# Kernel optimization log

Measured on AMD Instinct MI355X. Metric: run time of the kernel, lower is better.

The kernel has to match this reference:

```python
import jax, jax.numpy as jnp
import numpy as np
from jax import lax


def setup_inputs() -> dict:
    key = jax.random.key(0)
    k1, k2, k3, k4 = jax.random.split(key, 4)
    D = 128
    B = 16
    image = jax.random.normal(k1, (1, D, D, D), jnp.float32)          # [1, D, H, W]
    x = jax.random.normal(k2, (B, 1, D, D, D), jnp.float32)           # [B, 1, D, H, W]
    # Conv3d(1, 27, kernel_size=3) parameters
    W = jax.random.normal(k3, (27, 1, 3, 3, 3), jnp.float32) * (1.0 / np.sqrt(27.0))
    b = jax.random.normal(k4, (27,), jnp.float32) * 0.01
    return {"image": image, "x": x, "W": W, "b": b}


def reference(image, x, W, b):
    D, H, Wd = image.shape[1], image.shape[2], image.shape[3]
    # K = Conv3d(image): per-voxel 27 filter taps. Unbatched CDHW -> add batch dim.
    K = lax.conv_general_dilated(
        image[None], W, window_strides=(1, 1, 1), padding='SAME',
        dimension_numbers=('NCDHW', 'OIDHW', 'NCDHW'))[0]             # [27, D, H, W]
    K = K + b[:, None, None, None]
    # permute (1,2,3,0) + unflatten(3,(3,3,3)) -> [D, H, W, 3, 3, 3]
    K = jnp.moveaxis(K, 0, -1).reshape(D, H, Wd, 3, 3, 3)
    # Apply dynamic per-voxel 3x3x3 filter: sum of 27 shifted slices
    xp = jnp.pad(x, ((0, 0), (0, 0), (1, 1), (1, 1), (1, 1)))         # [B,1,D+2,H+2,W+2]
    y = jnp.zeros_like(x)
    for di in range(3):
        for dj in range(3):
            for dk in range(3):
                tap = K[..., di, dj, dk][None, None]                  # [1,1,D,H,W]
                y = y + tap * xp[:, :, di:di + D, dj:dj + H, dk:dk + Wd]
    return y
```

## Files before the change

### kernel.cpp

```cpp
#include <hip/hip_runtime.h>

typedef __fp16 f16x2 __attribute__((ext_vector_type(2)));

#define Dm 128
#define Bn 16
#define VOX (Dm * Dm * Dm)
#define NT 256
#define WR 10
#define SLAB 320

__device__ __forceinline__ int iclamp(int v, int lo, int hi) {
  return v < lo ? lo : (v > hi ? hi : v);
}
__device__ __forceinline__ f16x2 pkrtz(float lo, float hi) {
  return __builtin_amdgcn_cvt_pkrtz(lo, hi);
}
__device__ __forceinline__ float pkbits(float lo, float hi) {
  return __builtin_bit_cast(float, __builtin_amdgcn_cvt_pkrtz(lo, hi));
}
__device__ __forceinline__ f16x2 asf16x2(float w) {
  return __builtin_bit_cast(f16x2, w);
}
__device__ __forceinline__ f16x2 midpair(f16x2 P, f16x2 Q) {
  unsigned r = __builtin_amdgcn_perm(__builtin_bit_cast(unsigned, P),
                                     __builtin_bit_cast(unsigned, Q),
                                     0x05040302u);
  return __builtin_bit_cast(f16x2, r);
}

extern "C" __global__ void packW(const float* __restrict__ Wf,
                                 const float* __restrict__ bfp,
                                 float* __restrict__ wpk) {
  int i = threadIdx.x;
  if (i < 729) {
    int o = i / 27, t = i - o * 27;
    float v = Wf[i];
    wpk[t * 27 + o] = pkbits(v, v);
  } else if (i < 756) {
    float b = bfp[i - 729];
    wpk[i] = pkbits(b, b);
  }
}

__device__ __forceinline__ void load_batch(float2 nx[5], const float* xb,
                                           const int off[5]) {
#pragma unroll
  for (int k = 0; k < 5; ++k) nx[k] = *(const float2*)(xb + off[k]);
}
__device__ __forceinline__ void stage_lds(float* sxw, const float2 nx[5],
                                          int lane) {
#pragma unroll
  for (int k = 0; k < 5; ++k)
    sxw[64 * k + lane] = pkbits(nx[k].x, nx[k].y);
}
__device__ __forceinline__ f16x2 apply_tile(const float* sxw, const f16x2* K2,
                                            int ty, int tx) {
  f16x2 aA = {(__fp16)0.f, (__fp16)0.f};
  f16x2 aB = {(__fp16)0.f, (__fp16)0.f};
#pragma unroll
  for (int rr = 0; rr < 9; ++rr) {
    const int idx = ((rr / 3) * 10 + ty + (rr % 3)) * WR + tx;
    f16x2 a2 = asf16x2(sxw[idx]);
    f16x2 b2 = asf16x2(sxw[idx + 1]);
    f16x2 c2 = asf16x2(sxw[idx + 2]);
    f16x2 h01 = midpair(b2, a2);
    f16x2 h12 = b2;
    f16x2 h23 = midpair(c2, b2);
    if (rr & 1) {
      aB = __builtin_elementwise_fma(K2[rr * 3 + 0], h01, aB);
      aB = __builtin_elementwise_fma(K2[rr * 3 + 1], h12, aB);
      aB = __builtin_elementwise_fma(K2[rr * 3 + 2], h23, aB);
    } else {
      aA = __builtin_elementwise_fma(K2[rr * 3 + 0], h01, aA);
      aA = __builtin_elementwise_fma(K2[rr * 3 + 1], h12, aA);
      aA = __builtin_elementwise_fma(K2[rr * 3 + 2], h23, aA);
    }
  }
  return aA + aB;
}

extern "C" __global__ void __launch_bounds__(NT, 4)
fused3d(const float* __restrict__ img, const float* __restrict__ x,
        const float* __restrict__ wpk, float* __restrict__ out)
{
  __shared__ float sImg[4][SLAB];
  __shared__ float sX0[4][SLAB];
  __shared__ float sX1[4][SLAB];

  const int tid  = threadIdx.x;
  const int lane = tid & 63;
  const int wv   = tid >> 6;
  const int tx   = lane & 7;
  const int ty   = lane >> 3;

  const int bid = blockIdx.x;
  const int s  = (bid & 7) * 512 + (bid >> 3);
  const int bx = s & 7, by = (s >> 3) & 15, bz = s >> 7;
  const int w0 = bx * 16, h0 = by * 8, d0 = bz * 4;

  int off[5];
  float mk0[5], mk1[5];
#pragma unroll
  for (int k = 0; k < 5; ++k) {
    int i  = 64 * k + lane;
    int r  = i / WR;
    int c  = i - r * WR;
    int zz = r / 10;
    int yy = r - zz * 10;
    int gdo = d0 + wv + zz - 1;
    int gho = h0 + yy - 1;
    int gwo = w0 - 2 + 2 * c;
    int gd = iclamp(gdo, 0, Dm - 1);
    int gh = iclamp(gho, 0, Dm - 1);
    int gw = iclamp(gwo, 0, Dm - 2);
    off[k] = (gd * Dm + gh) * Dm + gw;
    bool rk = ((unsigned)gdo < Dm) & ((unsigned)gho < Dm);
    mk0[k] = (rk & ((unsigned)gwo < Dm))       ? 1.f : 0.f;
    mk1[k] = (rk & ((unsigned)(gwo + 1) < Dm)) ? 1.f : 0.f;
  }

  float* simg = sImg[wv];
  float* sx0  = sX0[wv];
  float* sx1  = sX1[wv];

  float2 nxA[5], nxB[5];
  load_batch(nxA, x, off);
#pragma unroll
  for (int k = 0; k < 5; ++k) {
    float2 v = *(const float2*)(img + off[k]);
    simg[64 * k + lane] = pkbits(v.x * mk0[k], v.y * mk1[k]);
  }

  f16x2 K2[27];
#pragma unroll
  for (int o = 0; o < 27; ++o) K2[o] = asf16x2(wpk[729 + o]);
#pragma unroll
  for (int rr = 0; rr < 9; ++rr) {
    const int idx = ((rr / 3) * 10 + ty + (rr % 3)) * WR + tx;
    f16x2 a2 = asf16x2(simg[idx]);
    f16x2 b2 = asf16x2(simg[idx + 1]);
    f16x2 c2 = asf16x2(simg[idx + 2]);
    f16x2 h01 = midpair(b2, a2);
    f16x2 h12 = b2;
    f16x2 h23 = midpair(c2, b2);
    const float* wA = wpk + (rr * 3 + 0) * 27;
    const float* wB = wpk + (rr * 3 + 1) * 27;
    const float* wC = wpk + (rr * 3 + 2) * 27;
#pragma unroll
    for (int o = 0; o < 27; ++o) {
      K2[o] = __builtin_elementwise_fma(asf16x2(wA[o]), h01, K2[o]);
      K2[o] = __builtin_elementwise_fma(asf16x2(wB[o]), h12, K2[o]);
      K2[o] = __builtin_elementwise_fma(asf16x2(wC[o]), h23, K2[o]);
    }
  }

  const int od = d0 + wv, oh = h0 + ty, ow = w0 + 2 * tx;
#pragma unroll
  for (int o = 0; o < 27; ++o) {
    const int di = o / 9, dj = (o / 3) % 3, dk = o % 3;
    const bool mm = ((unsigned)(od + di - 1) < Dm) & ((unsigned)(oh + dj - 1) < Dm);
    const float m0 = (mm & ((unsigned)(ow + dk - 1) < Dm)) ? 1.f : 0.f;
    const float m1 = (mm & ((unsigned)(ow + dk)     < Dm)) ? 1.f : 0.f;
    K2[o] *= pkrtz(m0, m1);
  }

  const size_t obase = (((size_t)od) * Dm + oh) * Dm + ow;

#pragma unroll 1
  for (int bb = 0; bb < Bn; bb += 2) {
    stage_lds(sx0, nxA, lane);
    load_batch(nxB, x + (size_t)(bb + 1) * VOX, off);
    {
      f16x2 acc = apply_tile(sx0, K2, ty, tx);
      float2 st; st.x = (float)acc.x; st.y = (float)acc.y;
      *(float2*)&out[(size_t)bb * VOX + obase] = st;
    }
    stage_lds(sx1, nxB, lane);
    if (bb + 2 < Bn) load_batch(nxA, x + (size_t)(bb + 2) * VOX, off);
    {
      f16x2 acc = apply_tile(sx1, K2, ty, tx);
      float2 st; st.x = (float)acc.x; st.y = (float)acc.y;
      *(float2*)&out[(size_t)(bb + 1) * VOX + obase] = st;
    }
  }
}

extern "C" void kernel_launch(void* const* d_in, const int* in_sizes, int n_in,
                              void* d_out, int out_size, void* d_ws, size_t ws_size,
                              hipStream_t stream) {
  const float* img = (const float*)d_in[0];
  const float* x   = (const float*)d_in[1];
  const float* Wf  = (const float*)d_in[2];
  const float* bf  = (const float*)d_in[3];
  float* out = (float*)d_out;
  float* wpk = (float*)d_ws;
  hipLaunchKernelGGL(packW, dim3(1), dim3(768), 0, stream, Wf, bf, wpk);
  hipLaunchKernelGGL(fused3d, dim3(4096), dim3(NT), 0, stream, img, x, wpk, out);
}
```

Before: 122.2 us.

## Compute four output voxels per thread with wider tiles and float4 stores

Each thread now produces four consecutive W outputs instead of two, so the block tile widens to 32 and the grid is halved. Per-thread dynamic kernels double to two register sets (KA, KB), sharing LDS loads and midpair shuffles across both pairs. The image slab LDS buffer is dropped and sX0 is reused for the initial K computation. The aim is fewer LDS reads per output and wider stores, at the cost of higher register pressure (54 packed kernel registers plus 9 prefetch float2 per buffer) and less parallelism.

```diff
diff --git a/kernel.cpp b/kernel.cpp
--- a/kernel.cpp
+++ b/kernel.cpp
@@ -6,8 +6,9 @@
 #define Bn 16
 #define VOX (Dm * Dm * Dm)
 #define NT 256
-#define WR 10
-#define SLAB 320
+#define WR 19
+#define SLAB 589
+#define NSL 9
 
 __device__ __forceinline__ int iclamp(int v, int lo, int hi) {
   return v < lo ? lo : (v > hi ? hi : v);
@@ -42,48 +43,56 @@
   }
 }
 
-__device__ __forceinline__ void load_batch(float2 nx[5], const float* xb,
-                                           const int off[5]) {
-#pragma unroll
-  for (int k = 0; k < 5; ++k) nx[k] = *(const float2*)(xb + off[k]);
-}
-__device__ __forceinline__ void stage_lds(float* sxw, const float2 nx[5],
+__device__ __forceinline__ void load_batch(float2 nx[NSL], const float* xb,
+                                           const int off[NSL]) {
+#pragma unroll
+  for (int k = 0; k < NSL; ++k) nx[k] = *(const float2*)(xb + off[k]);
+}
+__device__ __forceinline__ void stage_lds(float* sxw, const float2 nx[NSL],
                                           int lane) {
 #pragma unroll
-  for (int k = 0; k < 5; ++k)
+  for (int k = 0; k < NSL; ++k)
     sxw[64 * k + lane] = pkbits(nx[k].x, nx[k].y);
 }
-__device__ __forceinline__ f16x2 apply_tile(const float* sxw, const f16x2* K2,
-                                            int ty, int tx) {
-  f16x2 aA = {(__fp16)0.f, (__fp16)0.f};
-  f16x2 aB = {(__fp16)0.f, (__fp16)0.f};
+
+__device__ __forceinline__ void apply_tile4(const float* sxw,
+                                            const f16x2* KA, const f16x2* KB,
+                                            int ty, int tx,
+                                            f16x2& outA, f16x2& outB) {
+  f16x2 aAa = {(__fp16)0.f, (__fp16)0.f}, aAb = aAa;
+  f16x2 aBa = aAa, aBb = aAa;
 #pragma unroll
   for (int rr = 0; rr < 9; ++rr) {
-    const int idx = ((rr / 3) * 10 + ty + (rr % 3)) * WR + tx;
-    f16x2 a2 = asf16x2(sxw[idx]);
-    f16x2 b2 = asf16x2(sxw[idx + 1]);
-    f16x2 c2 = asf16x2(sxw[idx + 2]);
-    f16x2 h01 = midpair(b2, a2);
-    f16x2 h12 = b2;
-    f16x2 h23 = midpair(c2, b2);
+    const int idx = ((rr / 3) * 10 + ty + (rr % 3)) * WR + 2 * tx;
+    float u0 = sxw[idx], u1 = sxw[idx + 1], u2 = sxw[idx + 2], u3 = sxw[idx + 3];
+    f16x2 h1 = asf16x2(u1), h2 = asf16x2(u2);
+    f16x2 m01 = midpair(h1, asf16x2(u0));
+    f16x2 m12 = midpair(h2, h1);
+    f16x2 m23 = midpair(asf16x2(u3), h2);
     if (rr & 1) {
-      aB = __builtin_elementwise_fma(K2[rr * 3 + 0], h01, aB);
-      aB = __builtin_elementwise_fma(K2[rr * 3 + 1], h12, aB);
-      aB = __builtin_elementwise_fma(K2[rr * 3 + 2], h23, aB);
+      aAb = __builtin_elementwise_fma(KA[rr * 3 + 0], m01, aAb);
+      aAb = __builtin_elementwise_fma(KA[rr * 3 + 1], h1,  aAb);
+      aAb = __builtin_elementwise_fma(KA[rr * 3 + 2], m12, aAb);
+      aBb = __builtin_elementwise_fma(KB[rr * 3 + 0], m12, aBb);
+      aBb = __builtin_elementwise_fma(KB[rr * 3 + 1], h2,  aBb);
+      aBb = __builtin_elementwise_fma(KB[rr * 3 + 2], m23, aBb);
     } else {
-      aA = __builtin_elementwise_fma(K2[rr * 3 + 0], h01, aA);
-      aA = __builtin_elementwise_fma(K2[rr * 3 + 1], h12, aA);
-      aA = __builtin_elementwise_fma(K2[rr * 3 + 2], h23, aA);
-    }
-  }
-  return aA + aB;
+      aAa = __builtin_elementwise_fma(KA[rr * 3 + 0], m01, aAa);
+      aAa = __builtin_elementwise_fma(KA[rr * 3 + 1], h1,  aAa);
+      aAa = __builtin_elementwise_fma(KA[rr * 3 + 2], m12, aAa);
+      aBa = __builtin_elementwise_fma(KB[rr * 3 + 0], m12, aBa);
+      aBa = __builtin_elementwise_fma(KB[rr * 3 + 1], h2,  aBa);
+      aBa = __builtin_elementwise_fma(KB[rr * 3 + 2], m23, aBa);
+    }
+  }
+  outA = aAa + aAb;
+  outB = aBa + aBb;
 }
 
 extern "C" __global__ void __launch_bounds__(NT, 4)
 fused3d(const float* __restrict__ img, const float* __restrict__ x,
         const float* __restrict__ wpk, float* __restrict__ out)
 {
-  __shared__ float sImg[4][SLAB];
   __shared__ float sX0[4][SLAB];
   __shared__ float sX1[4][SLAB];
 
@@ -94,14 +103,14 @@
   const int ty   = lane >> 3;
 
   const int bid = blockIdx.x;
-  const int s  = (bid & 7) * 512 + (bid >> 3);
-  const int bx = s & 7, by = (s >> 3) & 15, bz = s >> 7;
-  const int w0 = bx * 16, h0 = by * 8, d0 = bz * 4;
-
-  int off[5];
-  float mk0[5], mk1[5];
-#pragma unroll
-  for (int k = 0; k < 5; ++k) {
+  const int s  = (bid & 7) * 256 + (bid >> 3);
+  const int bx = s & 3, by = (s >> 2) & 15, bz = s >> 6;
+  const int w0 = bx * 32, h0 = by * 8, d0 = bz * 4;
+
+  int off[NSL];
+  float mk0[NSL], mk1[NSL];
+#pragma unroll
+  for (int k = 0; k < NSL; ++k) {
     int i  = 64 * k + lane;
     int r  = i / WR;
     int c  = i - r * WR;
@@ -114,73 +123,82 @@
     int gh = iclamp(gho, 0, Dm - 1);
     int gw = iclamp(gwo, 0, Dm - 2);
     off[k] = (gd * Dm + gh) * Dm + gw;
-    bool rk = ((unsigned)gdo < Dm) & ((unsigned)gho < Dm);
+    bool rk = ((unsigned)gdo < Dm) & ((unsigned)gho < Dm) & (zz < 3);
     mk0[k] = (rk & ((unsigned)gwo < Dm))       ? 1.f : 0.f;
     mk1[k] = (rk & ((unsigned)(gwo + 1) < Dm)) ? 1.f : 0.f;
   }
 
-  float* simg = sImg[wv];
-  float* sx0  = sX0[wv];
-  float* sx1  = sX1[wv];
-
-  float2 nxA[5], nxB[5];
+  float* sx0 = sX0[wv];
+  float* sx1 = sX1[wv];
+
+  float2 nxA[NSL], nxB[NSL];
   load_batch(nxA, x, off);
 #pragma unroll
-  for (int k = 0; k < 5; ++k) {
+  for (int k = 0; k < NSL; ++k) {
     float2 v = *(const float2*)(img + off[k]);
-    simg[64 * k + lane] = pkbits(v.x * mk0[k], v.y * mk1[k]);
-  }
-
-  f16x2 K2[27];
-#pragma unroll
-  for (int o = 0; o < 27; ++o) K2[o] = asf16x2(wpk[729 + o]);
+    sx0[64 * k + lane] = pkbits(v.x * mk0[k], v.y * mk1[k]);
+  }
+
+  f16x2 KA[27], KB[27];
+#pragma unroll
+  for (int o = 0; o < 27; ++o) { KA[o] = asf16x2(wpk[729 + o]); KB[o] = KA[o]; }
 #pragma unroll
   for (int rr = 0; rr < 9; ++rr) {
-    const int idx = ((rr / 3) * 10 + ty + (rr % 3)) * WR + tx;
-    f16x2 a2 = asf16x2(simg[idx]);
-    f16x2 b2 = asf16x2(simg[idx + 1]);
-    f16x2 c2 = asf16x2(simg[idx + 2]);
-    f16x2 h01 = midpair(b2, a2);
-    f16x2 h12 = b2;
-    f16x2 h23 = midpair(c2, b2);
+    const int idx = ((rr / 3) * 10 + ty + (rr % 3)) * WR + 2 * tx;
+    float u0 = sx0[idx], u1 = sx0[idx + 1], u2 = sx0[idx + 2], u3 = sx0[idx + 3];
+    f16x2 h1 = asf16x2(u1), h2 = asf16x2(u2);
+    f16x2 m01 = midpair(h1, asf16x2(u0));
+    f16x2 m12 = midpair(h2, h1);
+    f16x2 m23 = midpair(asf16x2(u3), h2);
     const float* wA = wpk + (rr * 3 + 0) * 27;
     const float* wB = wpk + (rr * 3 + 1) * 27;
     const float* wC = wpk + (rr * 3 + 2) * 27;
 #pragma unroll
     for (int o = 0; o < 27; ++o) {
-      K2[o] = __builtin_elementwise_fma(asf16x2(wA[o]), h01, K2[o]);
-      K2[o] = __builtin_elementwise_fma(asf16x2(wB[o]), h12, K2[o]);
-      K2[o] = __builtin_elementwise_fma(asf16x2(wC[o]), h23, K2[o]);
-    }
-  }
-
-  const int od = d0 + wv, oh = h0 + ty, ow = w0 + 2 * tx;
+      f16x2 wa = asf16x2(wA[o]), wb = asf16x2(wB[o]), wc = asf16x2(wC[o]);
+      KA[o] = __builtin_elementwise_fma(wa, m01, KA[o]);
+      KA[o] = __builtin_elementwise_fma(wb, h1,  KA[o]);
+      KA[o] = __builtin_elementwise_fma(wc, m12, KA[o]);
+      KB[o] = __builtin_elementwise_fma(wa, m12, KB[o]);
+      KB[o] = __builtin_elementwise_fma(wb, h2,  KB[o]);
+      KB[o] = __builtin_elementwise_fma(wc, m23, KB[o]);
+    }
+  }
+
+  const int od = d0 + wv, oh = h0 + ty, ow = w0 + 4 * tx;
 #pragma unroll
   for (int o = 0; o < 27; ++o) {
     const int di = o / 9, dj = (o / 3) % 3, dk = o % 3;
     const bool mm = ((unsigned)(od + di - 1) < Dm) & ((unsigned)(oh + dj - 1) < Dm);
-    const float m0 = (mm & ((unsigned)(ow + dk - 1) < Dm)) ? 1.f : 0.f;
-    const float m1 = (mm & ((unsigned)(ow + dk)     < Dm)) ? 1.f : 0.f;
-    K2[o] *= pkrtz(m0, m1);
+    const float a0 = (mm & ((unsigned)(ow + dk - 1) < Dm)) ? 1.f : 0.f;
+    const float a1 = (mm & ((unsigned)(ow + dk)     < Dm)) ? 1.f : 0.f;
+    const float b0 = (mm & ((unsigned)(ow + dk + 1) < Dm)) ? 1.f : 0.f;
+    const float b1 = (mm & ((unsigned)(ow + dk + 2) < Dm)) ? 1.f : 0.f;
+    KA[o] *= pkrtz(a0, a1);
+    KB[o] *= pkrtz(b0, b1);
   }
 
   const size_t obase = (((size_t)od) * Dm + oh) * Dm + ow;
 
 #pragma unroll 1
   for (int bb = 0; bb < Bn; bb += 2) {
-    stage_lds(sx0, nxA, lane);
+    stage_lds(sx1, nxA, lane);
     load_batch(nxB, x + (size_t)(bb + 1) * VOX, off);
     {
-      f16x2 acc = apply_tile(sx0, K2, ty, tx);
-      float2 st; st.x = (float)acc.x; st.y = (float)acc.y;
-      *(float2*)&out[(size_t)bb * VOX + obase] = st;
-    }
-    stage_lds(sx1, nxB, lane);
+      f16x2 oA, oB;
+      apply_tile4(sx1, KA, KB, ty, tx, oA, oB);
+      float4 st; st.x = (float)oA.x; st.y = (float)oA.y;
+      st.z = (float)oB.x; st.w = (float)oB.y;
+      *(float4*)&out[(size_t)bb * VOX + obase] = st;
+    }
+    stage_lds(sx0, nxB, lane);
     if (bb + 2 < Bn) load_batch(nxA, x + (size_t)(bb + 2) * VOX, off);
     {
-      f16x2 acc = apply_tile(sx1, K2, ty, tx);
-      float2 st; st.x = (float)acc.x; st.y = (float)acc.y;
-      *(float2*)&out[(size_t)(bb + 1) * VOX + obase] = st;
+      f16x2 oA, oB;
+      apply_tile4(sx0, KA, KB, ty, tx, oA, oB);
+      float4 st; st.x = (float)oA.x; st.y = (float)oA.y;
+      st.z = (float)oB.x; st.w = (float)oB.y;
+      *(float4*)&out[(size_t)(bb + 1) * VOX + obase] = st;
     }
   }
 }
@@ -195,5 +213,5 @@
   float* out = (float*)d_out;
   float* wpk = (float*)d_ws;
   hipLaunchKernelGGL(packW, dim3(1), dim3(768), 0, stream, Wf, bf, wpk);
-  hipLaunchKernelGGL(fused3d, dim3(4096), dim3(NT), 0, stream, img, x, wpk, out);
-}
+  hipLaunchKernelGGL(fused3d, dim3(2048), dim3(NT), 0, stream, img, x, wpk, out);
+}
```

New measurement: 133.5 us. 9.2% more time.
